# Optimization experiments

Measured on AMD Instinct MI355X. Metric: run time of the kernel, lower is better.

## Reference

```python
import jax, jax.numpy as jnp
import numpy as np

K = 3       # kernel size
STRIDE = 1
PAD = 1
BN_EPS = 1e-5


def setup_inputs() -> dict:
    key = jax.random.key(0)
    ks = jax.random.split(key, 5)
    B, C, H, W = 4, 64, 128, 128
    OC = 64
    x = jax.random.normal(ks[0], (B, C, H, W), dtype=jnp.float32)
    # offset conv weights scaled small so predicted offsets are a few pixels
    w_off = jax.random.normal(ks[1], (2 * K * K, C, K, K), dtype=jnp.float32) * 0.01
    b_off = jnp.zeros((2 * K * K,), dtype=jnp.float32)
    fan_in = C * K * K
    w_def = jax.random.normal(ks[2], (OC, C, K, K), dtype=jnp.float32) / np.sqrt(fan_in)
    b_def = jnp.zeros((OC,), dtype=jnp.float32)
    gamma = jnp.ones((OC,), dtype=jnp.float32)
    beta = jnp.zeros((OC,), dtype=jnp.float32)
    prelu_w = jnp.full((OC,), 0.2, dtype=jnp.float32)  # nn.PReLU(init=0.2)
    return {"x": x, "w_off": w_off, "b_off": b_off, "w_def": w_def,
            "b_def": b_def, "gamma": gamma, "beta": beta, "prelu_w": prelu_w}


def _conv2d(x, w, b):
    out = jax.lax.conv_general_dilated(
        x, w, window_strides=(STRIDE, STRIDE),
        padding=[(PAD, PAD), (PAD, PAD)],
        dimension_numbers=("NCHW", "OIHW", "NCHW"))
    return out + b[None, :, None, None]


def _deform_conv(x, offset, w, b):
    """torchvision-style deform_conv2d (groups=1, no modulation)."""
    B, C, H, W = x.shape
    OC = w.shape[0]
    Ho, Wo = offset.shape[2], offset.shape[3]
    kk = K * K
    off = offset.reshape(B, kk, 2, Ho, Wo)
    dy, dx = off[:, :, 0], off[:, :, 1]                 # [B,kk,Ho,Wo]
    kh = (jnp.arange(kk) // K).astype(jnp.float32)
    kw = (jnp.arange(kk) % K).astype(jnp.float32)
    ys = (jnp.arange(Ho) * STRIDE - PAD).astype(jnp.float32)
    xs = (jnp.arange(Wo) * STRIDE - PAD).astype(jnp.float32)
    py = ys[None, None, :, None] + kh[None, :, None, None] + dy   # [B,kk,Ho,Wo]
    px = xs[None, None, None, :] + kw[None, :, None, None] + dx

    y0 = jnp.floor(py); x0 = jnp.floor(px)
    wy1 = py - y0; wy0 = 1.0 - wy1
    wx1 = px - x0; wx0 = 1.0 - wx1
    x_flat = x.reshape(B, C, H * W)

    def corner(yf, xf, wgt):
        yi = yf.astype(jnp.int32); xi = xf.astype(jnp.int32)
        valid = (yi >= 0) & (yi < H) & (xi >= 0) & (xi < W)
        yi = jnp.clip(yi, 0, H - 1); xi = jnp.clip(xi, 0, W - 1)
        idx = (yi * W + xi).reshape(B, 1, -1)           # [B,1,kk*Ho*Wo]
        vals = jnp.take_along_axis(x_flat, idx, axis=2)  # [B,C,kk*Ho*Wo]
        wm = (wgt * valid.astype(wgt.dtype)).reshape(B, 1, -1)
        return vals * wm

    samp = (corner(y0, x0, wy0 * wx0) + corner(y0, x0 + 1, wy0 * wx1)
            + corner(y0 + 1, x0, wy1 * wx0) + corner(y0 + 1, x0 + 1, wy1 * wx1))
    samp = samp.reshape(B, C, kk, Ho, Wo)
    out = jnp.einsum("bckhw,ock->bohw", samp, w.reshape(OC, C, kk))
    return out + b[None, :, None, None]


def reference(x, w_off, b_off, w_def, b_def, gamma, beta, prelu_w):
    offset = _conv2d(x, w_off, b_off)
    y = _deform_conv(x, offset, w_def, b_def)
    # BatchNorm2d (training-mode batch stats)
    mean = jnp.mean(y, axis=(0, 2, 3), keepdims=True)
    var = jnp.var(y, axis=(0, 2, 3), keepdims=True)
    y = (y - mean) * jax.lax.rsqrt(var + BN_EPS)
    y = y * gamma[None, :, None, None] + beta[None, :, None, None]
    # PReLU per-channel
    return jnp.where(y >= 0, y, prelu_w[None, :, None, None] * y)
```

## Files before the change

### kernel.cpp

```cpp
#include <hip/hip_runtime.h>

#define BSZ 4
#define CIN 64
#define HH 128
#define WW 128
#define OCH 64
#define HWSZ (HH*WW)
#define KK 9
#define NPIX (BSZ*HH*WW)

typedef __attribute__((ext_vector_type(8))) short short8v;
typedef __attribute__((ext_vector_type(8))) unsigned short ushort8v;
typedef __attribute__((ext_vector_type(4))) float float4v;

#define Y_OFF     0
#define WTB_OFF   2097152
#define WOFB_OFF  (WTB_OFF + 18432)
#define STATS_OFF (WOFB_OFF + 9216)

__device__ __forceinline__ short f2bf(float f) {
    unsigned u = __builtin_bit_cast(unsigned, f);
    unsigned r = (u + 0x7FFFu + ((u >> 16) & 1u)) >> 16;
    return (short)r;
}
__device__ __forceinline__ float bf2f(unsigned short u) {
    return __builtin_bit_cast(float, ((unsigned)u) << 16);
}

__global__ void prep_w(const float* __restrict__ w_def,
                       const float* __restrict__ w_off,
                       short* __restrict__ wtb,
                       short* __restrict__ wofb,
                       float* __restrict__ stats) {
    int i = blockIdx.x * 256 + threadIdx.x;
    if (blockIdx.x == 0 && threadIdx.x < 128) stats[threadIdx.x] = 0.f;
    if (i < 36864) {
        int oc = i / 576, rr = i % 576;
        int c = rr / 9, k = rr % 9;
        wtb[(k * OCH + oc) * CIN + c] = f2bf(w_def[i]);
    } else if (i < 36864 + 18432) {
        int j = i - 36864;
        int o = j / 576, rr = j % 576;
        int tap = rr / 64, c = rr % 64;
        wofb[j] = (o < 18) ? f2bf(w_off[(o * 64 + c) * 9 + tap]) : (short)0;
    }
}

__global__ __launch_bounds__(256, 8) void transpose_x(const float* __restrict__ x,
                                                      unsigned short* __restrict__ xt) {
    __shared__ float t[64][33];
    const int bid = blockIdx.x;
    const int wg  = (bid & 7) * 256 + (bid >> 3);
    const int tid = threadIdx.x;
    const int gp0 = wg * 32;
    const int b   = gp0 >> 14;
    const int hw0 = gp0 & 16383;
    const float* src = x + b * CIN * HWSZ + hw0;
    #pragma unroll
    for (int pass = 0; pass < 8; ++pass) {
        int c = pass * 8 + (tid >> 5);
        int p = tid & 31;
        t[c][p] = src[c * HWSZ + p];
    }
    __syncthreads();
    unsigned short* dst = xt + (b * HWSZ + hw0) * 64;
    #pragma unroll
    for (int pass = 0; pass < 8; ++pass) {
        int p = pass * 4 + (tid >> 6);
        int c = tid & 63;
        dst[p * 64 + c] = (unsigned short)f2bf(t[c][p]);
    }
}

__global__ __launch_bounds__(256, 2) void deform_fused(
    const unsigned short* __restrict__ xt,
    const short* __restrict__ wofb,
    const float* __restrict__ b_off,
    const short* __restrict__ wtb,
    const float* __restrict__ b_def,
    unsigned short* __restrict__ ybuf,
    float* __restrict__ gsum,
    float* __restrict__ gsq)
{
    __shared__ unsigned short band[6 * 80 * 64];
    __shared__ float off_lds[18][64];
    __shared__ float red0[4][64];
    __shared__ float red1[4][64];

    const int bid  = blockIdx.x;
    const int r    = (bid & 7) * 128 + (bid >> 3);
    const int tid  = threadIdx.x;
    const int lane = tid & 63;
    const int wv   = tid >> 6;
    const int b    = r >> 8;
    const int rem  = r & 255;
    const int ho   = rem >> 1, half = rem & 1;
    const int l15  = lane & 15;
    const int l4   = lane >> 4;
    const int cbase = l4 * 8;
    const int p    = half * 64 + wv * 16 + l15;
    const int wx0  = half * 64 - 8;

    const unsigned short* xb = xt + b * HWSZ * 64;
    char* bandc = (char*)band;

    #pragma unroll
    for (int i = 0; i < 15; ++i) {
        int G  = i * 256 + tid;
        int g  = G & 7;
        int xs = (G >> 3) % 80;
        int rs = G / 640;
        int row = min(max(ho - 2 + rs, 0), HH - 1);
        int col = min(max(wx0 + xs, 0), WW - 1);
        ushort8v v = *(const ushort8v*)(xb + (row * WW + col) * 64 + g * 8);
        int dstB = ((rs * 80 + xs) << 7) + ((g ^ (xs & 7)) << 4);
        *(ushort8v*)(bandc + dstB) = v;
    }
    __syncthreads();

    {
        float4v offacc0 = (float4v){0.f, 0.f, 0.f, 0.f};
        float4v offacc1 = (float4v){0.f, 0.f, 0.f, 0.f};
        const ushort8v zero8 = {0, 0, 0, 0, 0, 0, 0, 0};
        #pragma unroll
        for (int kk = 0; kk < 18; ++kk) {
            const int tap = kk >> 1;
            const int kh = tap / 3, kw = tap % 3;
            const int yy = ho - 1 + kh;
            const int xx = p - 1 + kw;
            const bool valid = ((unsigned)yy < (unsigned)HH) & ((unsigned)xx < (unsigned)WW);
            ushort8v bo = zero8;
            if (valid) {
                int xs = xx - wx0;
                int q  = l4 + (kk & 1) * 4;
                int adr = (((kh + 1) * 80 + xs) << 7) + ((q ^ (xs & 7)) << 4);
                bo = *(const ushort8v*)(bandc + adr);
            }
            short8v bos = __builtin_bit_cast(short8v, bo);
            short8v af0 = *(const short8v*)(wofb + (l15) * 576 + kk * 32 + cbase);
            short8v af1 = *(const short8v*)(wofb + (16 + l15) * 576 + kk * 32 + cbase);
            offacc0 = __builtin_amdgcn_mfma_f32_16x16x32_bf16(af0, bos, offacc0, 0, 0, 0);
            offacc1 = __builtin_amdgcn_mfma_f32_16x16x32_bf16(af1, bos, offacc1, 0, 0, 0);
        }
        const int col = wv * 16 + l15;
        #pragma unroll
        for (int rr = 0; rr < 4; ++rr) {
            int row = l4 * 4 + rr;
            off_lds[row][col] = offacc0[rr] + b_off[row];
        }
        if (l4 == 0) {
            #pragma unroll
            for (int rr = 0; rr < 2; ++rr) {
                int row = 16 + rr;
                off_lds[row][col] = offacc1[rr] + b_off[row];
            }
        }
    }
    __syncthreads();

    float och[18];
    {
        const int col = wv * 16 + l15;
        #pragma unroll
        for (int j = 0; j < 18; ++j) och[j] = off_lds[j][col];
    }

    float4v acc[4];
    #pragma unroll
    for (int mt = 0; mt < 4; ++mt) acc[mt] = (float4v){0.f, 0.f, 0.f, 0.f};

    #pragma unroll
    for (int k = 0; k < KK; ++k) {
        float dy = och[2 * k];
        float dx = och[2 * k + 1];
        float py = (float)(ho - 1 + (k / 3)) + dy;
        float px = (float)(p - 1 + (k % 3)) + dx;
        float y0f = floorf(py), x0f = floorf(px);
        int y0 = (int)y0f, x0 = (int)x0f;
        float wy1 = py - y0f, wy0 = 1.f - wy1;
        float wx1 = px - x0f, wx0f_ = 1.f - wx1;
        int vy0 = ((unsigned)y0 < (unsigned)HH), vy1 = ((unsigned)(y0 + 1) < (unsigned)HH);
        int vx0 = ((unsigned)x0 < (unsigned)WW), vx1 = ((unsigned)(x0 + 1) < (unsigned)WW);
        float w00 = wy0 * wx0f_ * (float)(vy0 & vx0);
        float w01 = wy0 * wx1  * (float)(vy0 & vx1);
        float w10 = wy1 * wx0f_ * (float)(vy1 & vx0);
        float w11 = wy1 * wx1  * (float)(vy1 & vx1);
        int y0c = min(max(y0, 0), HH - 1), y1c = min(max(y0 + 1, 0), HH - 1);
        int x0c = min(max(x0, 0), WW - 1), x1c = min(max(x0 + 1, 0), WW - 1);

        int sy0 = y0c - (ho - 2), sy1 = y1c - (ho - 2);
        int sx0 = x0c - wx0,      sx1 = x1c - wx0;
        bool inb = (sy0 >= 0) & (sy1 < 6) & (sx0 >= 0) & (sx1 < 80);

        ushort8v g00a, g01a, g10a, g11a, g00b, g01b, g10b, g11b;
        if (__builtin_expect(inb, 1)) {
            const int qa = l4, qb = l4 + 4;
            int a00 = ((sy0 * 80 + sx0) << 7);
            int a01 = ((sy0 * 80 + sx1) << 7);
            int a10 = ((sy1 * 80 + sx0) << 7);
            int a11 = ((sy1 * 80 + sx1) << 7);
            int h0 = (sx0 & 7), h1 = (sx1 & 7);
            g00a = *(const ushort8v*)(bandc + a00 + ((qa ^ h0) << 4));
            g01a = *(const ushort8v*)(bandc + a01 + ((qa ^ h1) << 4));
            g10a = *(const ushort8v*)(bandc + a10 + ((qa ^ h0) << 4));
            g11a = *(const ushort8v*)(bandc + a11 + ((qa ^ h1) << 4));
            g00b = *(const ushort8v*)(bandc + a00 + ((qb ^ h0) << 4));
            g01b = *(const ushort8v*)(bandc + a01 + ((qb ^ h1) << 4));
            g10b = *(const ushort8v*)(bandc + a10 + ((qb ^ h0) << 4));
            g11b = *(const ushort8v*)(bandc + a11 + ((qb ^ h1) << 4));
        } else {
            const unsigned short* p00 = xb + (y0c * WW + x0c) * 64 + cbase;
            const unsigned short* p01 = xb + (y0c * WW + x1c) * 64 + cbase;
            const unsigned short* p10 = xb + (y1c * WW + x0c) * 64 + cbase;
            const unsigned short* p11 = xb + (y1c * WW + x1c) * 64 + cbase;
            g00a = *(const ushort8v*)(p00);      g01a = *(const ushort8v*)(p01);
            g10a = *(const ushort8v*)(p10);      g11a = *(const ushort8v*)(p11);
            g00b = *(const ushort8v*)(p00 + 32); g01b = *(const ushort8v*)(p01 + 32);
            g10b = *(const ushort8v*)(p10 + 32); g11b = *(const ushort8v*)(p11 + 32);
        }

        short8v Bf[2];
        #pragma unroll
        for (int j = 0; j < 8; ++j) {
            float v = bf2f(g00a[j]) * w00 + bf2f(g01a[j]) * w01
                    + bf2f(g10a[j]) * w10 + bf2f(g11a[j]) * w11;
            Bf[0][j] = f2bf(v);
        }
        #pragma unroll
        for (int j = 0; j < 8; ++j) {
            float v = bf2f(g00b[j]) * w00 + bf2f(g01b[j]) * w01
                    + bf2f(g10b[j]) * w10 + bf2f(g11b[j]) * w11;
            Bf[1][j] = f2bf(v);
        }

        const short* wk = wtb + k * OCH * CIN;
        #pragma unroll
        for (int mt = 0; mt < 4; ++mt) {
            const short* wrow = wk + (mt * 16 + l15) * CIN + cbase;
            #pragma unroll
            for (int kc = 0; kc < 2; ++kc) {
                short8v Af = *(const short8v*)(wrow + kc * 32);
                acc[mt] = __builtin_amdgcn_mfma_f32_16x16x32_bf16(Af, Bf[kc], acc[mt], 0, 0, 0);
            }
        }
    }

    float lsum[4][4], lsq[4][4];
    const int yrow = ho * WW;
    #pragma unroll
    for (int mt = 0; mt < 4; ++mt) {
        #pragma unroll
        for (int rr = 0; rr < 4; ++rr) {
            const int oc = mt * 16 + l4 * 4 + rr;
            float v = acc[mt][rr] + b_def[oc];
            ybuf[(b * OCH + oc) * HWSZ + yrow + p] = (unsigned short)f2bf(v);
            lsum[mt][rr] = v;
            lsq[mt][rr]  = v * v;
        }
    }
    #pragma unroll
    for (int m = 1; m <= 8; m <<= 1) {
        #pragma unroll
        for (int mt = 0; mt < 4; ++mt)
            #pragma unroll
            for (int rr = 0; rr < 4; ++rr) {
                lsum[mt][rr] += __shfl_xor(lsum[mt][rr], m);
                lsq[mt][rr]  += __shfl_xor(lsq[mt][rr], m);
            }
    }
    if (l15 == 0) {
        #pragma unroll
        for (int mt = 0; mt < 4; ++mt)
            #pragma unroll
            for (int rr = 0; rr < 4; ++rr) {
                const int oc = mt * 16 + l4 * 4 + rr;
                red0[wv][oc] = lsum[mt][rr];
                red1[wv][oc] = lsq[mt][rr];
            }
    }
    __syncthreads();
    if (tid < 128) {
        const int oc = tid & 63, s = tid >> 6;
        if (s == 0) {
            float v = red0[0][oc] + red0[1][oc] + red0[2][oc] + red0[3][oc];
            atomicAdd(&gsum[oc], v);
        } else {
            float v = red1[0][oc] + red1[1][oc] + red1[2][oc] + red1[3][oc];
            atomicAdd(&gsq[oc], v);
        }
    }
}

__global__ void finalize_bn(const float* __restrict__ gsum, const float* __restrict__ gsq,
                            const float* __restrict__ gamma, const float* __restrict__ beta,
                            float* __restrict__ ss) {
    int c = threadIdx.x;
    if (c < OCH) {
        const float inv = 1.f / (float)NPIX;
        float mean = gsum[c] * inv;
        float var = gsq[c] * inv - mean * mean;
        float rstd = rsqrtf(var + 1e-5f);
        float sc = gamma[c] * rstd;
        ss[c] = sc;
        ss[OCH + c] = beta[c] - mean * sc;
    }
}

__global__ __launch_bounds__(256) void apply_bn(const unsigned short* __restrict__ ybuf,
                                                const float* __restrict__ ss,
                                                const float* __restrict__ prelu,
                                                float* __restrict__ out) {
    int i = blockIdx.x * 256 + threadIdx.x;
    int oc = ((i * 8) >> 14) & 63;
    float sc = ss[oc], sh = ss[OCH + oc], pw = prelu[oc];
    ushort8v v8 = ((const ushort8v*)ybuf)[i];
    float4 o0, o1;
    float t;
    t = fmaf(bf2f(v8[0]), sc, sh); o0.x = t >= 0.f ? t : pw * t;
    t = fmaf(bf2f(v8[1]), sc, sh); o0.y = t >= 0.f ? t : pw * t;
    t = fmaf(bf2f(v8[2]), sc, sh); o0.z = t >= 0.f ? t : pw * t;
    t = fmaf(bf2f(v8[3]), sc, sh); o0.w = t >= 0.f ? t : pw * t;
    t = fmaf(bf2f(v8[4]), sc, sh); o1.x = t >= 0.f ? t : pw * t;
    t = fmaf(bf2f(v8[5]), sc, sh); o1.y = t >= 0.f ? t : pw * t;
    t = fmaf(bf2f(v8[6]), sc, sh); o1.z = t >= 0.f ? t : pw * t;
    t = fmaf(bf2f(v8[7]), sc, sh); o1.w = t >= 0.f ? t : pw * t;
    ((float4*)out)[i * 2]     = o0;
    ((float4*)out)[i * 2 + 1] = o1;
}

extern "C" void kernel_launch(void* const* d_in, const int* in_sizes, int n_in,
                              void* d_out, int out_size, void* d_ws, size_t ws_size,
                              hipStream_t stream) {
    const float* x      = (const float*)d_in[0];
    const float* w_off  = (const float*)d_in[1];
    const float* b_off  = (const float*)d_in[2];
    const float* w_def  = (const float*)d_in[3];
    const float* b_def  = (const float*)d_in[4];
    const float* gamma  = (const float*)d_in[5];
    const float* beta   = (const float*)d_in[6];
    const float* prelu  = (const float*)d_in[7];

    float* ws    = (float*)d_ws;
    unsigned short* ybuf = (unsigned short*)(ws + Y_OFF);
    short* wtb   = (short*)(ws + WTB_OFF);
    short* wofb  = (short*)(ws + WOFB_OFF);
    float* stats = ws + STATS_OFF;
    float* gsum  = stats;
    float* gsq   = stats + OCH;
    float* ss    = stats + 2 * OCH;

    unsigned short* xt = (unsigned short*)d_out;

    prep_w<<<216, 256, 0, stream>>>(w_def, w_off, wtb, wofb, stats);
    transpose_x<<<BSZ * HWSZ / 32, 256, 0, stream>>>(x, xt);
    deform_fused<<<BSZ * HH * 2, 256, 0, stream>>>(xt, wofb, b_off, wtb, b_def, ybuf, gsum, gsq);
    finalize_bn<<<1, 64, 0, stream>>>(gsum, gsq, gamma, beta, ss);
    apply_bn<<<(BSZ * OCH * HWSZ) / 8 / 256, 256, 0, stream>>>(ybuf, ss, prelu, (float*)d_out);
}
```

Measured before the change: 173.9 us.

## Merge prep kernels, fold BN finalize into apply, shrink LDS band for occupancy

Merges weight prep and the x transpose into one launch, and folds the BN finalize step into apply_bn, removing two kernel launches. In deform_fused the LDS input band shrinks from 80 to 70 columns. The offset values now move between lanes by shuffles rather than through an LDS array, and the stat reduction reuses the band memory. Together these cut shared memory so launch bounds can ask for 3 blocks per CU. The cost is fewer halo columns for large offsets, which sends more samples to the out-of-band path, plus redundant per-thread BN scale math in apply_bn.

Result: no change. 173.6 us (-0.2%).

```diff
diff --git a/kernel.cpp b/kernel.cpp
--- a/kernel.cpp
+++ b/kernel.cpp
@@ -27,31 +27,32 @@
     return __builtin_bit_cast(float, ((unsigned)u) << 16);
 }
 
-__global__ void prep_w(const float* __restrict__ w_def,
-                       const float* __restrict__ w_off,
-                       short* __restrict__ wtb,
-                       short* __restrict__ wofb,
-                       float* __restrict__ stats) {
-    int i = blockIdx.x * 256 + threadIdx.x;
-    if (blockIdx.x == 0 && threadIdx.x < 128) stats[threadIdx.x] = 0.f;
-    if (i < 36864) {
-        int oc = i / 576, rr = i % 576;
-        int c = rr / 9, k = rr % 9;
-        wtb[(k * OCH + oc) * CIN + c] = f2bf(w_def[i]);
-    } else if (i < 36864 + 18432) {
-        int j = i - 36864;
-        int o = j / 576, rr = j % 576;
-        int tap = rr / 64, c = rr % 64;
-        wofb[j] = (o < 18) ? f2bf(w_off[(o * 64 + c) * 9 + tap]) : (short)0;
-    }
-}
-
-__global__ __launch_bounds__(256, 8) void transpose_x(const float* __restrict__ x,
-                                                      unsigned short* __restrict__ xt) {
+__global__ __launch_bounds__(256) void prep(const float* __restrict__ x,
+                                            const float* __restrict__ w_def,
+                                            const float* __restrict__ w_off,
+                                            unsigned short* __restrict__ xt,
+                                            short* __restrict__ wtb,
+                                            short* __restrict__ wofb,
+                                            float* __restrict__ stats) {
     __shared__ float t[64][33];
     const int bid = blockIdx.x;
+    const int tid = threadIdx.x;
+    if (bid >= 2048) {
+        if (bid == 2048 && tid < 128) stats[tid] = 0.f;
+        int i = (bid - 2048) * 256 + tid;
+        if (i < 36864) {
+            int oc = i / 576, rr = i % 576;
+            int c = rr / 9, k = rr % 9;
+            wtb[(k * OCH + oc) * CIN + c] = f2bf(w_def[i]);
+        } else if (i < 36864 + 18432) {
+            int j = i - 36864;
+            int o = j / 576, rr = j % 576;
+            int tap = rr / 64, c = rr % 64;
+            wofb[j] = (o < 18) ? f2bf(w_off[(o * 64 + c) * 9 + tap]) : (short)0;
+        }
+        return;
+    }
     const int wg  = (bid & 7) * 256 + (bid >> 3);
-    const int tid = threadIdx.x;
     const int gp0 = wg * 32;
     const int b   = gp0 >> 14;
     const int hw0 = gp0 & 16383;
@@ -72,7 +73,7 @@
     }
 }
 
-__global__ __launch_bounds__(256, 2) void deform_fused(
+__global__ __launch_bounds__(256, 3) void deform_fused(
     const unsigned short* __restrict__ xt,
     const short* __restrict__ wofb,
     const float* __restrict__ b_off,
@@ -82,10 +83,7 @@
     float* __restrict__ gsum,
     float* __restrict__ gsq)
 {
-    __shared__ unsigned short band[6 * 80 * 64];
-    __shared__ float off_lds[18][64];
-    __shared__ float red0[4][64];
-    __shared__ float red1[4][64];
+    __shared__ unsigned short band[6 * 70 * 64];
 
     const int bid  = blockIdx.x;
     const int r    = (bid & 7) * 128 + (bid >> 3);
@@ -99,25 +97,27 @@
     const int l4   = lane >> 4;
     const int cbase = l4 * 8;
     const int p    = half * 64 + wv * 16 + l15;
-    const int wx0  = half * 64 - 8;
+    const int bx0  = half * 64 - 3;
 
     const unsigned short* xb = xt + b * HWSZ * 64;
     char* bandc = (char*)band;
 
     #pragma unroll
-    for (int i = 0; i < 15; ++i) {
-        int G  = i * 256 + tid;
-        int g  = G & 7;
-        int xs = (G >> 3) % 80;
-        int rs = G / 640;
-        int row = min(max(ho - 2 + rs, 0), HH - 1);
-        int col = min(max(wx0 + xs, 0), WW - 1);
-        ushort8v v = *(const ushort8v*)(xb + (row * WW + col) * 64 + g * 8);
-        int dstB = ((rs * 80 + xs) << 7) + ((g ^ (xs & 7)) << 4);
-        *(ushort8v*)(bandc + dstB) = v;
+    for (int i = 0; i < 14; ++i) {
+        int G = i * 256 + tid;
+        if (G < 3360) {
+            int g  = G & 7;
+            int xs = (G >> 3) % 70;
+            int rs = (G >> 3) / 70;
+            int row = min(max(ho - 2 + rs, 0), HH - 1);
+            int col = min(max(bx0 + xs, 0), WW - 1);
+            ushort8v v = *(const ushort8v*)(xb + (row * WW + col) * 64 + g * 8);
+            *(ushort8v*)(bandc + ((rs * 70 + xs) << 7) + ((g ^ (xs & 7)) << 4)) = v;
+        }
     }
     __syncthreads();
 
+    float och[18];
     {
         float4v offacc0 = (float4v){0.f, 0.f, 0.f, 0.f};
         float4v offacc1 = (float4v){0.f, 0.f, 0.f, 0.f};
@@ -131,9 +131,9 @@
             const bool valid = ((unsigned)yy < (unsigned)HH) & ((unsigned)xx < (unsigned)WW);
             ushort8v bo = zero8;
             if (valid) {
-                int xs = xx - wx0;
+                int xs = xx - bx0;
                 int q  = l4 + (kk & 1) * 4;
-                int adr = (((kh + 1) * 80 + xs) << 7) + ((q ^ (xs & 7)) << 4);
+                int adr = (((kh + 1) * 70 + xs) << 7) + ((q ^ (xs & 7)) << 4);
                 bo = *(const ushort8v*)(bandc + adr);
             }
             short8v bos = __builtin_bit_cast(short8v, bo);
@@ -142,27 +142,12 @@
             offacc0 = __builtin_amdgcn_mfma_f32_16x16x32_bf16(af0, bos, offacc0, 0, 0, 0);
             offacc1 = __builtin_amdgcn_mfma_f32_16x16x32_bf16(af1, bos, offacc1, 0, 0, 0);
         }
-        const int col = wv * 16 + l15;
-        #pragma unroll
-        for (int rr = 0; rr < 4; ++rr) {
-            int row = l4 * 4 + rr;
-            off_lds[row][col] = offacc0[rr] + b_off[row];
-        }
-        if (l4 == 0) {
-            #pragma unroll
-            for (int rr = 0; rr < 2; ++rr) {
-                int row = 16 + rr;
-                off_lds[row][col] = offacc1[rr] + b_off[row];
-            }
-        }
-    }
-    __syncthreads();
-
-    float och[18];
-    {
-        const int col = wv * 16 + l15;
-        #pragma unroll
-        for (int j = 0; j < 18; ++j) och[j] = off_lds[j][col];
+        #pragma unroll
+        for (int j = 0; j < 16; ++j)
+            och[j] = __shfl(offacc0[j & 3], (j >> 2) * 16 + l15) + b_off[j];
+        #pragma unroll
+        for (int t2 = 0; t2 < 2; ++t2)
+            och[16 + t2] = __shfl(offacc1[t2], l15) + b_off[16 + t2];
     }
 
     float4v acc[4];
@@ -189,16 +174,16 @@
         int x0c = min(max(x0, 0), WW - 1), x1c = min(max(x0 + 1, 0), WW - 1);
 
         int sy0 = y0c - (ho - 2), sy1 = y1c - (ho - 2);
-        int sx0 = x0c - wx0,      sx1 = x1c - wx0;
-        bool inb = (sy0 >= 0) & (sy1 < 6) & (sx0 >= 0) & (sx1 < 80);
+        int sx0 = x0c - bx0,      sx1 = x1c - bx0;
+        bool inb = (sy0 >= 0) & (sy1 < 6) & (sx0 >= 0) & (sx1 < 70);
 
         ushort8v g00a, g01a, g10a, g11a, g00b, g01b, g10b, g11b;
         if (__builtin_expect(inb, 1)) {
             const int qa = l4, qb = l4 + 4;
-            int a00 = ((sy0 * 80 + sx0) << 7);
-            int a01 = ((sy0 * 80 + sx1) << 7);
-            int a10 = ((sy1 * 80 + sx0) << 7);
-            int a11 = ((sy1 * 80 + sx1) << 7);
+            int a00 = ((sy0 * 70 + sx0) << 7);
+            int a01 = ((sy0 * 70 + sx1) << 7);
+            int a10 = ((sy1 * 70 + sx0) << 7);
+            int a11 = ((sy1 * 70 + sx1) << 7);
             int h0 = (sx0 & 7), h1 = (sx1 & 7);
             g00a = *(const ushort8v*)(bandc + a00 + ((qa ^ h0) << 4));
             g01a = *(const ushort8v*)(bandc + a01 + ((qa ^ h1) << 4));
@@ -268,51 +253,43 @@
                 lsq[mt][rr]  += __shfl_xor(lsq[mt][rr], m);
             }
     }
+    __syncthreads();
+    float* redp = (float*)bandc;
     if (l15 == 0) {
         #pragma unroll
         for (int mt = 0; mt < 4; ++mt)
             #pragma unroll
             for (int rr = 0; rr < 4; ++rr) {
                 const int oc = mt * 16 + l4 * 4 + rr;
-                red0[wv][oc] = lsum[mt][rr];
-                red1[wv][oc] = lsq[mt][rr];
+                redp[(0 * 4 + wv) * 64 + oc] = lsum[mt][rr];
+                redp[(1 * 4 + wv) * 64 + oc] = lsq[mt][rr];
             }
     }
     __syncthreads();
     if (tid < 128) {
         const int oc = tid & 63, s = tid >> 6;
-        if (s == 0) {
-            float v = red0[0][oc] + red0[1][oc] + red0[2][oc] + red0[3][oc];
-            atomicAdd(&gsum[oc], v);
-        } else {
-            float v = red1[0][oc] + red1[1][oc] + red1[2][oc] + red1[3][oc];
-            atomicAdd(&gsq[oc], v);
-        }
-    }
-}
-
-__global__ void finalize_bn(const float* __restrict__ gsum, const float* __restrict__ gsq,
-                            const float* __restrict__ gamma, const float* __restrict__ beta,
-                            float* __restrict__ ss) {
-    int c = threadIdx.x;
-    if (c < OCH) {
-        const float inv = 1.f / (float)NPIX;
-        float mean = gsum[c] * inv;
-        float var = gsq[c] * inv - mean * mean;
-        float rstd = rsqrtf(var + 1e-5f);
-        float sc = gamma[c] * rstd;
-        ss[c] = sc;
-        ss[OCH + c] = beta[c] - mean * sc;
+        float v = redp[(s * 4 + 0) * 64 + oc] + redp[(s * 4 + 1) * 64 + oc]
+                + redp[(s * 4 + 2) * 64 + oc] + redp[(s * 4 + 3) * 64 + oc];
+        atomicAdd((s == 0) ? &gsum[oc] : &gsq[oc], v);
     }
 }
 
 __global__ __launch_bounds__(256) void apply_bn(const unsigned short* __restrict__ ybuf,
-                                                const float* __restrict__ ss,
+                                                const float* __restrict__ gsum,
+                                                const float* __restrict__ gsq,
+                                                const float* __restrict__ gamma,
+                                                const float* __restrict__ beta,
                                                 const float* __restrict__ prelu,
                                                 float* __restrict__ out) {
     int i = blockIdx.x * 256 + threadIdx.x;
     int oc = ((i * 8) >> 14) & 63;
-    float sc = ss[oc], sh = ss[OCH + oc], pw = prelu[oc];
+    const float inv = 1.f / (float)NPIX;
+    float mean = gsum[oc] * inv;
+    float var  = gsq[oc] * inv - mean * mean;
+    float rstd = rsqrtf(var + 1e-5f);
+    float sc = gamma[oc] * rstd;
+    float sh = beta[oc] - mean * sc;
+    float pw = prelu[oc];
     ushort8v v8 = ((const ushort8v*)ybuf)[i];
     float4 o0, o1;
     float t;
@@ -347,13 +324,10 @@
     float* stats = ws + STATS_OFF;
     float* gsum  = stats;
     float* gsq   = stats + OCH;
-    float* ss    = stats + 2 * OCH;
 
     unsigned short* xt = (unsigned short*)d_out;
 
-    prep_w<<<216, 256, 0, stream>>>(w_def, w_off, wtb, wofb, stats);
-    transpose_x<<<BSZ * HWSZ / 32, 256, 0, stream>>>(x, xt);
+    prep<<<2048 + 216, 256, 0, stream>>>(x, w_def, w_off, xt, wtb, wofb, stats);
     deform_fused<<<BSZ * HH * 2, 256, 0, stream>>>(xt, wofb, b_off, wtb, b_def, ybuf, gsum, gsq);
-    finalize_bn<<<1, 64, 0, stream>>>(gsum, gsq, gamma, beta, ss);
-    apply_bn<<<(BSZ * OCH * HWSZ) / 8 / 256, 256, 0, stream>>>(ybuf, ss, prelu, (float*)d_out);
-}
+    apply_bn<<<(BSZ * OCH * HWSZ) / 8 / 256, 256, 0, stream>>>(ybuf, gsum, gsq, gamma, beta, prelu, (float*)d_out);
+}
```
